# Kernel optimization log

Hardware: AMD Instinct MI355X
Metric: run time of the kernel (lower is better)

Reference implementation:

```python
import jax, jax.numpy as jnp
import numpy as np

N_ROLES = 6
EPS = 1e-5

def _ln(x, scale, bias):
    m = jnp.mean(x, axis=-1, keepdims=True)
    v = jnp.var(x, axis=-1, keepdims=True)
    return (x - m) * jax.lax.rsqrt(v + EPS) * scale + bias

def setup_inputs() -> dict:
    key = jax.random.key(0)
    ks = jax.random.split(key, 20)
    T, B, D_OBS, H, A = 32, 1024, 256, 512, 32
    inp = {
        'rnn_states': jax.random.normal(ks[0], (B, H), jnp.float32),
        'obs': jax.random.normal(ks[1], (T, B, D_OBS), jnp.float32),
        'resets': jnp.zeros((T, B), jnp.float32),
        'available_actions': jnp.ones((T, B, A), jnp.float32),
        'role_ids': jax.random.randint(ks[2], (T, B), 0, N_ROLES, jnp.int32),
        # feature norm over obs_dim
        'fn_scale': jnp.ones((D_OBS,), jnp.float32),
        'fn_bias': jnp.zeros((D_OBS,), jnp.float32),
        # base MLP: obs_dim->512->512, each followed by LayerNorm
        'W0': jax.random.normal(ks[3], (D_OBS, H), jnp.float32) * 0.02,
        'b0': jnp.zeros((H,), jnp.float32),
        'ln0_scale': jnp.ones((H,), jnp.float32),
        'ln0_bias': jnp.zeros((H,), jnp.float32),
        'W1': jax.random.normal(ks[4], (H, H), jnp.float32) * 0.02,
        'b1': jnp.zeros((H,), jnp.float32),
        'ln1_scale': jnp.ones((H,), jnp.float32),
        'ln1_bias': jnp.zeros((H,), jnp.float32),
        # per-role routes: obs_dim->128->H (stacked over roles)
        'Wr0': jax.random.normal(ks[5], (N_ROLES, D_OBS, 128), jnp.float32) * 0.02,
        'br0': jnp.zeros((N_ROLES, 128), jnp.float32),
        'Wr1': jax.random.normal(ks[6], (N_ROLES, 128, H), jnp.float32) * 0.02,
        'br1': jnp.zeros((N_ROLES, H), jnp.float32),
        # per-role heads: H->64->32->action_dim (stacked over roles)
        'Wh0': jax.random.normal(ks[7], (N_ROLES, H, 64), jnp.float32) * 0.02,
        'bh0': jnp.zeros((N_ROLES, 64), jnp.float32),
        'Wh1': jax.random.normal(ks[8], (N_ROLES, 64, 32), jnp.float32) * 0.02,
        'bh1': jnp.zeros((N_ROLES, 32), jnp.float32),
        'Wh2': jax.random.normal(ks[9], (N_ROLES, 32, A), jnp.float32) * 0.02,
        'bh2': jnp.zeros((N_ROLES, A), jnp.float32),
    }
    return inp

def _gather_by_role(all_values, role_ids):
    # all_values: (K, T, B, F); role_ids: (T, B) -> (T, B, F)
    idx = role_ids[None, :, :, None].astype(jnp.int32)
    return jnp.take_along_axis(all_values, idx, axis=0)[0]

def reference(rnn_states, obs, resets, available_actions, role_ids,
              fn_scale, fn_bias, W0, b0, ln0_scale, ln0_bias,
              W1, b1, ln1_scale, ln1_bias,
              Wr0, br0, Wr1, br1,
              Wh0, bh0, Wh1, bh1, Wh2, bh2):
    # feature normalization on raw obs
    obs_n = _ln(obs, fn_scale, fn_bias)
    # shared base MLP (relu + LayerNorm after each Dense)
    e = _ln(jax.nn.relu(obs_n @ W0 + b0), ln0_scale, ln0_bias)
    e = _ln(jax.nn.relu(e @ W1 + b1), ln1_scale, ln1_bias)
    # per-role pre-GRU residual routes on (normalized) obs
    r = jax.nn.relu(jnp.einsum('tbi,kih->ktbh', obs_n, Wr0) + br0[:, None, None, :])
    r = jax.nn.relu(jnp.einsum('ktbh,kho->ktbo', r, Wr1) + br1[:, None, None, :])
    e = e + _gather_by_role(r, role_ids)
    # no recurrent policy configured: rnn_states pass through
    # per-role heads -> all logits (K, T, B, A)
    h = jax.nn.relu(jnp.einsum('tbh,khf->ktbf', e, Wh0) + bh0[:, None, None, :])
    h = jax.nn.relu(jnp.einsum('ktbf,kfg->ktbg', h, Wh1) + bh1[:, None, None, :])
    all_logits = jnp.einsum('ktbg,kga->ktba', h, Wh2) + bh2[:, None, None, :]
    logits = _gather_by_role(all_logits, role_ids)
    logits = jnp.where(available_actions > 0.5, logits, jnp.full_like(logits, -1e10))
    return rnn_states, logits
```

## Files before the change

### kernel.cpp

```cpp
#include <hip/hip_runtime.h>
#include <stdint.h>

typedef unsigned short u16;
typedef unsigned int u32;

using bf16x8 = __attribute__((ext_vector_type(8))) short;
using f32x4  = __attribute__((ext_vector_type(4))) float;

#define DEVINL __device__ __forceinline__

DEVINL float b2f(u16 u) { return __builtin_bit_cast(float, (u32)u << 16); }
DEVINL u16 f2b(float f) {
  u32 u = __builtin_bit_cast(u32, f);
  u += 0x7FFFu + ((u >> 16) & 1u);
  return (u16)(u >> 16);
}

DEVINL void gll16(const u16* src, u16* dst) {
  __builtin_amdgcn_global_load_lds(
      (const __attribute__((address_space(1))) void*)(uintptr_t)src,
      (__attribute__((address_space(3))) void*)(uintptr_t)dst, 16, 0, 0);
}

#define MFMA __builtin_amdgcn_mfma_f32_16x16x32_bf16
#define NROLE 6

__global__ __launch_bounds__(256) void role_count(
    const int* __restrict__ rid, int* __restrict__ blkCnt)
{
  __shared__ int h[NROLE];
  if (threadIdx.x < NROLE) h[threadIdx.x] = 0;
  __syncthreads();
  atomicAdd(&h[rid[blockIdx.x * 256 + threadIdx.x]], 1);
  __syncthreads();
  if (threadIdx.x < NROLE) blkCnt[blockIdx.x * NROLE + threadIdx.x] = h[threadIdx.x];
}

__global__ __launch_bounds__(256) void fill2(
    const int* __restrict__ rid, const int* __restrict__ blkCnt,
    int* __restrict__ bucket, int* __restrict__ baseArr, int* __restrict__ cntArr)
{
  __shared__ int c[128 * NROLE];
  __shared__ int preArr[NROLE], scnt[NROLE], sbase[NROLE], h[NROLE];
  const int tid = threadIdx.x;
  const int bx = blockIdx.x;
  for (int i = tid; i < 128 * NROLE; i += 256) c[i] = blkCnt[i];
  if (tid < NROLE) h[tid] = 0;
  __syncthreads();
  if (tid < NROLE) {
    int k = tid, run = 0, pre = 0;
    for (int b = 0; b < 128; ++b) { if (b == bx) pre = run; run += c[b * NROLE + k]; }
    scnt[k] = run; preArr[k] = pre;
  }
  __syncthreads();
  if (tid == 0) {
    int r = 0;
    for (int k = 0; k < NROLE; ++k) { sbase[k] = r; r += scnt[k]; }
  }
  __syncthreads();
  if (bx == 0 && tid < NROLE) { baseArr[tid] = sbase[tid]; cntArr[tid] = scnt[tid]; }
  int i = bx * 256 + tid;
  int k = rid[i];
  int pos = atomicAdd(&h[k], 1);
  bucket[sbase[k] + preArr[k] + pos] = i;
}

DEVINL void tp_tile(const float* __restrict__ s, u16* __restrict__ d,
                    int R, int C, int bx, int by, int z)
{
  __shared__ u16 tile[32][33];
  const size_t mstride = (size_t)R * C;
  s += (size_t)z * mstride;
  d += (size_t)z * mstride;
  int r0 = bx * 32, c0 = by * 32;
  int tx = threadIdx.x & 31, ty = threadIdx.x >> 5;
#pragma unroll
  for (int i = 0; i < 32; i += 8)
    tile[ty + i][tx] = f2b(s[(size_t)(r0 + ty + i) * C + (c0 + tx)]);
  __syncthreads();
#pragma unroll
  for (int i = 0; i < 32; i += 8)
    d[(size_t)(c0 + ty + i) * R + (r0 + tx)] = tile[tx][ty + i];
}

__global__ __launch_bounds__(256) void mega0(
    const float* W0, const float* W1, const float* Wr0, const float* Wr1, const float* Wh0,
    u16* W0t, u16* W1t, u16* Wr0t, u16* Wr1t, u16* Wh0t,
    const float* __restrict__ obs, const float* __restrict__ fn_s,
    const float* __restrict__ fn_b, u16* __restrict__ obs_nB,
    const int* __restrict__ bucket,
    const float* __restrict__ rnn, float* __restrict__ outRnn)
{
  int b = blockIdx.x;
  const int tid = threadIdx.x;
  if (b < 1152) {
    if (b < 128)      {            tp_tile(W0, W0t, 256, 512, b % 8,  b / 8, 0); }
    else if (b < 384) { b -= 128;  tp_tile(W1, W1t, 512, 512, b % 16, b / 16, 0); }
    else if (b < 576) { b -= 384;  int t = b / 8;  tp_tile(Wr0, Wr0t, 256, 128, b % 8,  t % 4,  t / 4); }
    else if (b < 960) { b -= 576;  int t = b / 4;  tp_tile(Wr1, Wr1t, 128, 512, b % 4,  t % 16, t / 16); }
    else              { b -= 960;  int t = b / 16; tp_tile(Wh0, Wh0t, 512, 64,  b % 16, t % 2,  t / 2); }
  } else if (b < 3200) {
    b -= 1152;
    const int lane = tid & 63, wave = tid >> 6;
#pragma unroll
    for (int it = 0; it < 4; ++it) {
      int p = b * 16 + wave * 4 + it;
      int g = bucket[p];
      const float* xr = obs + (size_t)g * 256 + lane * 4;
      float x[4] __attribute__((aligned(16)));
      *(float4*)x = *(const float4*)xr;
      float s = 0.f, s2 = 0.f;
#pragma unroll
      for (int q = 0; q < 4; ++q) { s += x[q]; s2 += x[q] * x[q]; }
#pragma unroll
      for (int o = 32; o > 0; o >>= 1) { s += __shfl_xor(s, o, 64); s2 += __shfl_xor(s2, o, 64); }
      float m = s * (1.f / 256.f);
      float v = s2 * (1.f / 256.f) - m * m;
      float inv = rsqrtf(v + 1e-5f);
      u16 yu[4] __attribute__((aligned(8)));
#pragma unroll
      for (int q = 0; q < 4; ++q)
        yu[q] = f2b((x[q] - m) * inv * fn_s[lane * 4 + q] + fn_b[lane * 4 + q]);
      *(uint2*)(obs_nB + (size_t)p * 256 + lane * 4) = *(uint2*)yu;
    }
  } else {
    b -= 3200;
    const float4* src = (const float4*)rnn;
    float4* dst = (float4*)outRnn;
    int base = (b * 256 + tid) * 4;
#pragma unroll
    for (int i = 0; i < 4; ++i) dst[base + i] = src[base + i];
  }
}

template <int K>
__global__ __launch_bounds__(256, 2) void gemm_ln(
    const u16* __restrict__ A, const u16* __restrict__ Bt,
    const float* __restrict__ bias, const float* __restrict__ lnsc,
    const float* __restrict__ lnbi, u16* __restrict__ C)
{
  constexpr int BK = 64, NI = K / BK;
  __shared__ __align__(16) u16 As[2][64 * BK];
  __shared__ float redS[64][4];
  __shared__ float redSS[64][4];
  __shared__ float prm[1536];
  const int tid = threadIdx.x;
  const int rowBase = blockIdx.x * 64;
  const int lane = tid & 63, wave = tid >> 6;
#pragma unroll
  for (int i = tid; i < 512; i += 256) {
    prm[i] = bias[i]; prm[512 + i] = lnsc[i]; prm[1024 + i] = lnbi[i];
  }
  u32 aOff[2];
#pragma unroll
  for (int r = 0; r < 2; ++r) {
    int row = r * 32 + (tid >> 3);
    aOff[r] = (u32)(rowBase + row) * (u32)K + (u32)(((tid & 7) ^ (row & 7)) * 8);
  }
  const int quad = lane >> 4, lm = lane & 15, l7 = lm & 7;
  const int wn = wave * 128;
  u32 bOff[8];
#pragma unroll
  for (int j = 0; j < 8; ++j)
    bOff[j] = (u32)(wn + j * 16 + lm) * (u32)K + (u32)(quad * 8);

  f32x4 acc[4][8] = {};

#pragma unroll
  for (int r = 0; r < 2; ++r)
    gll16(A + aOff[r], &As[0][r * 2048 + wave * 512]);
  bf16x8 bP[8];
#pragma unroll
  for (int j = 0; j < 8; ++j)
    bP[j] = *(const bf16x8*)(Bt + bOff[j]);
  __syncthreads();

  for (int i = 0; i < NI; ++i) {
    const u16* Ab = As[i & 1];
    if (i + 1 < NI) {
#pragma unroll
      for (int r = 0; r < 2; ++r)
        gll16(A + aOff[r] + (i + 1) * BK, &As[(i + 1) & 1][r * 2048 + wave * 512]);
    }
    bf16x8 bN[8];
#pragma unroll
    for (int j = 0; j < 8; ++j)
      bN[j] = *(const bf16x8*)(Bt + bOff[j] + i * BK + 32);
    bf16x8 af[4];
#pragma unroll
    for (int i2 = 0; i2 < 4; ++i2)
      af[i2] = *(const bf16x8*)&Ab[(i2 * 16 + lm) * 64 + ((quad ^ l7) * 8)];
#pragma unroll
    for (int i2 = 0; i2 < 4; ++i2)
#pragma unroll
      for (int j = 0; j < 8; ++j)
        acc[i2][j] = MFMA(af[i2], bP[j], acc[i2][j], 0, 0, 0);
    if (i + 1 < NI) {
#pragma unroll
      for (int j = 0; j < 8; ++j)
        bP[j] = *(const bf16x8*)(Bt + bOff[j] + (i + 1) * BK);
    }
#pragma unroll
    for (int i2 = 0; i2 < 4; ++i2)
      af[i2] = *(const bf16x8*)&Ab[(i2 * 16 + lm) * 64 + (((quad + 4) ^ l7) * 8)];
#pragma unroll
    for (int i2 = 0; i2 < 4; ++i2)
#pragma unroll
      for (int j = 0; j < 8; ++j)
        acc[i2][j] = MFMA(af[i2], bN[j], acc[i2][j], 0, 0, 0);
    __syncthreads();
  }

#pragma unroll
  for (int i2 = 0; i2 < 4; ++i2) {
#pragma unroll
    for (int r2 = 0; r2 < 4; ++r2) {
      float s = 0.f, ss = 0.f;
#pragma unroll
      for (int j = 0; j < 8; ++j) {
        float v = fmaxf(acc[i2][j][r2] + prm[wn + j * 16 + lm], 0.f);
        acc[i2][j][r2] = v;
        s += v; ss += v * v;
      }
#pragma unroll
      for (int o = 1; o < 16; o <<= 1) { s += __shfl_xor(s, o, 64); ss += __shfl_xor(ss, o, 64); }
      if (lm == 0) {
        int rowL = i2 * 16 + quad * 4 + r2;
        redS[rowL][wave] = s;
        redSS[rowL][wave] = ss;
      }
    }
  }
  __syncthreads();
#pragma unroll
  for (int i2 = 0; i2 < 4; ++i2) {
#pragma unroll
    for (int r2 = 0; r2 < 4; ++r2) {
      int rowL = i2 * 16 + quad * 4 + r2;
      float ts  = redS[rowL][0] + redS[rowL][1] + redS[rowL][2] + redS[rowL][3];
      float tss = redSS[rowL][0] + redSS[rowL][1] + redSS[rowL][2] + redSS[rowL][3];
      float m = ts * (1.f / 512.f);
      float var = tss * (1.f / 512.f) - m * m;
      float inv = rsqrtf(var + 1e-5f);
      size_t base = (size_t)(rowBase + rowL) * 512;
#pragma unroll
      for (int j = 0; j < 8; ++j) {
        int col = wn + j * 16 + lm;
        float y = (acc[i2][j][r2] - m) * inv * prm[512 + col] + prm[1024 + col];
        C[base + col] = f2b(y);
      }
    }
  }
}

__global__ __launch_bounds__(256, 3) void route_head(
    const u16* __restrict__ obs_nB, const u16* __restrict__ e,
    const u16* __restrict__ Wr0t, const float* __restrict__ br0,
    const u16* __restrict__ Wr1t, const float* __restrict__ br1,
    const u16* __restrict__ Wh0t, const float* __restrict__ bh0,
    const float* __restrict__ Wh1, const float* __restrict__ bh1,
    const float* __restrict__ Wh2, const float* __restrict__ bh2,
    const float* __restrict__ avail,
    const int* __restrict__ bucket, const int* __restrict__ baseArr,
    const int* __restrict__ cntArr, float* __restrict__ outLogits)
{
  __shared__ __align__(16) u16 sm[24960];
  __shared__ float prm[704];
  const int tid = threadIdx.x;

  int role = 0, rem = blockIdx.x, cnt;
  for (;;) {
    cnt = cntArr[role];
    int tiles = (cnt + 31) >> 5;
    if (rem < tiles) break;
    rem -= tiles;
    if (++role >= NROLE) return;
  }
  const int limit = cnt;
  const int rowBase = rem * 32;
  const int roleBase = baseArr[role];

  const int lane = tid & 63, wave = tid >> 6;
  const int quad = lane >> 4, lm = lane & 15, l7 = lm & 7;

#pragma unroll
  for (int r = 0; r < 4; ++r) {
    int lrow = r * 8 + (tid >> 5);
    int i = rowBase + lrow;
    if (i >= limit) i = rowBase;
    gll16(obs_nB + (u32)(roleBase + i) * 256u + (u32)(((tid & 31) ^ (lrow & 7)) * 8),
          &sm[16384 + r * 2048 + wave * 512]);
  }
#pragma unroll
  for (int r = 0; r < 8; ++r) {
    int lrow = r * 4 + wave;
    int i = rowBase + lrow;
    if (i >= limit) i = rowBase;
    int chunk = tid & 63;
    int sw = (chunk & 56) | ((chunk ^ lrow) & 7);
    gll16(e + (u32)(roleBase + i) * 512u + (u32)(sw * 8), &sm[r * 2048 + wave * 512]);
  }
  {
    if (tid < 128) prm[tid] = br0[role * 128 + tid];
    for (int i = tid; i < 512; i += 256) prm[128 + i] = br1[role * 512 + i];
    if (tid < 64) prm[640 + tid] = bh0[role * 64 + tid];
  }
  __syncthreads();

  const int wn0 = wave * 32;
  const u16* B0 = Wr0t + (size_t)role * 128 * 256;
  f32x4 acc0[2][2] = {};
  bf16x8 b0R[2][2];
#pragma unroll
  for (int p = 0; p < 2; ++p)
#pragma unroll
    for (int j = 0; j < 2; ++j)
      b0R[p][j] = *(const bf16x8*)(B0 + (u32)(wn0 + j * 16 + lm) * 256u + (u32)(quad * 8 + p * 32));
#pragma unroll
  for (int it = 0; it < 8; ++it) {
    bf16x8 cur0 = b0R[it & 1][0], cur1 = b0R[it & 1][1];
    if (it + 2 < 8) {
#pragma unroll
      for (int j = 0; j < 2; ++j)
        b0R[it & 1][j] = *(const bf16x8*)(B0 + (u32)(wn0 + j * 16 + lm) * 256u + (u32)(quad * 8 + (it + 2) * 32));
    }
    const int kc = it * 4;
    bf16x8 af[2];
#pragma unroll
    for (int i2 = 0; i2 < 2; ++i2)
      af[i2] = *(const bf16x8*)&sm[16384 + (i2 * 16 + lm) * 256 + (((quad + kc) ^ l7) * 8)];
#pragma unroll
    for (int i2 = 0; i2 < 2; ++i2) {
      acc0[i2][0] = MFMA(af[i2], cur0, acc0[i2][0], 0, 0, 0);
      acc0[i2][1] = MFMA(af[i2], cur1, acc0[i2][1], 0, 0, 0);
    }
  }
  __syncthreads();
  u16* r1 = sm + 16384;
#pragma unroll
  for (int i2 = 0; i2 < 2; ++i2) {
#pragma unroll
    for (int r2 = 0; r2 < 4; ++r2) {
      int row = i2 * 16 + quad * 4 + r2;
#pragma unroll
      for (int j = 0; j < 2; ++j) {
        int col = wn0 + j * 16 + lm;
        float v = fmaxf(acc0[i2][j][r2] + prm[col], 0.f);
        r1[row * 128 + (((col >> 3) ^ (row & 7)) * 8) + (col & 7)] = f2b(v);
      }
    }
  }
  __syncthreads();

  const int wn1 = wave * 128;
  const u16* B1 = Wr1t + (size_t)role * 512 * 128;
  f32x4 acc1[2][8] = {};
  bf16x8 b1P[8];
#pragma unroll
  for (int j = 0; j < 8; ++j)
    b1P[j] = *(const bf16x8*)(B1 + (u32)(wn1 + j * 16 + lm) * 128u + (u32)(quad * 8));
#pragma unroll
  for (int kk = 0; kk < 128; kk += 32) {
    bf16x8 b1N[8];
    if (kk + 32 < 128) {
#pragma unroll
      for (int j = 0; j < 8; ++j)
        b1N[j] = *(const bf16x8*)(B1 + (u32)(wn1 + j * 16 + lm) * 128u + (u32)(quad * 8 + kk + 32));
    }
    const int kc = kk >> 3;
    bf16x8 af[2];
#pragma unroll
    for (int i2 = 0; i2 < 2; ++i2)
      af[i2] = *(const bf16x8*)&r1[(i2 * 16 + lm) * 128 + (((quad + kc) ^ l7) * 8)];
#pragma unroll
    for (int i2 = 0; i2 < 2; ++i2)
#pragma unroll
      for (int j = 0; j < 8; ++j)
        acc1[i2][j] = MFMA(af[i2], b1P[j], acc1[i2][j], 0, 0, 0);
    if (kk + 32 < 128) {
#pragma unroll
      for (int j = 0; j < 8; ++j) b1P[j] = b1N[j];
    }
  }
#pragma unroll
  for (int i2 = 0; i2 < 2; ++i2) {
#pragma unroll
    for (int r2 = 0; r2 < 4; ++r2) {
      int row = i2 * 16 + quad * 4 + r2;
#pragma unroll
      for (int j = 0; j < 8; ++j) {
        int col = wn1 + j * 16 + lm;
        int addr = row * 512 + (((col >> 3) ^ (row & 7)) * 8) + (col & 7);
        float v = fmaxf(acc1[i2][j][r2] + prm[128 + col], 0.f) + b2f(sm[addr]);
        sm[addr] = f2b(v);
      }
    }
  }
  __syncthreads();

  const int wn2 = wave * 16;
  const u16* B2 = Wh0t + (size_t)role * 64 * 512;
  f32x4 acc2[2] = {};
  bf16x8 b2R[4];
#pragma unroll
  for (int p = 0; p < 4; ++p)
    b2R[p] = *(const bf16x8*)(B2 + (u32)(wn2 + lm) * 512u + (u32)(quad * 8 + p * 32));
#pragma unroll
  for (int it = 0; it < 16; ++it) {
    bf16x8 cur = b2R[it & 3];
    if (it + 4 < 16)
      b2R[it & 3] = *(const bf16x8*)(B2 + (u32)(wn2 + lm) * 512u + (u32)(quad * 8 + (it + 4) * 32));
    const int kc = it * 4;
    bf16x8 af[2];
#pragma unroll
    for (int i2 = 0; i2 < 2; ++i2)
      af[i2] = *(const bf16x8*)&sm[(i2 * 16 + lm) * 512 + (((quad + kc) ^ l7) * 8)];
#pragma unroll
    for (int i2 = 0; i2 < 2; ++i2)
      acc2[i2] = MFMA(af[i2], cur, acc2[i2], 0, 0, 0);
  }
  u16* h0s = sm + 20480;
#pragma unroll
  for (int i2 = 0; i2 < 2; ++i2) {
#pragma unroll
    for (int r2 = 0; r2 < 4; ++r2) {
      int row = i2 * 16 + quad * 4 + r2;
      int col = wn2 + lm;
      h0s[row * 68 + col] = f2b(fmaxf(acc2[i2][r2] + prm[640 + col], 0.f));
    }
  }
  __syncthreads();

  {
    float* h1s = (float*)&sm[22656];
    const int r = tid >> 3;
    const int n0 = (tid & 7) * 4;
    const bool valid = (rowBase + r) < limit;
    const float* W1k = Wh1 + (size_t)role * 64 * 32;
    const float* W2k = Wh2 + (size_t)role * 32 * 32;
    float4 a1 = *(const float4*)(bh1 + role * 32 + n0);
#pragma unroll 8
    for (int j = 0; j < 64; ++j) {
      float hj = b2f(h0s[r * 68 + j]);
      float4 wv = *(const float4*)(W1k + j * 32 + n0);
      a1.x += hj * wv.x; a1.y += hj * wv.y; a1.z += hj * wv.z; a1.w += hj * wv.w;
    }
    h1s[r * 36 + n0 + 0] = fmaxf(a1.x, 0.f);
    h1s[r * 36 + n0 + 1] = fmaxf(a1.y, 0.f);
    h1s[r * 36 + n0 + 2] = fmaxf(a1.z, 0.f);
    h1s[r * 36 + n0 + 3] = fmaxf(a1.w, 0.f);
    __syncthreads();
    float4 a2 = *(const float4*)(bh2 + role * 32 + n0);
#pragma unroll 8
    for (int n = 0; n < 32; ++n) {
      float hn = h1s[r * 36 + n];
      float4 wv = *(const float4*)(W2k + n * 32 + n0);
      a2.x += hn * wv.x; a2.y += hn * wv.y; a2.z += hn * wv.z; a2.w += hn * wv.w;
    }
    if (valid) {
      int g = bucket[roleBase + rowBase + r];
      float4 av = *(const float4*)(avail + (size_t)g * 32 + n0);
      float4 o;
      o.x = (av.x > 0.5f) ? a2.x : -1e10f;
      o.y = (av.y > 0.5f) ? a2.y : -1e10f;
      o.z = (av.z > 0.5f) ? a2.z : -1e10f;
      o.w = (av.w > 0.5f) ? a2.w : -1e10f;
      *(float4*)(outLogits + (size_t)g * 32 + n0) = o;
    }
  }
}

extern "C" void kernel_launch(void* const* d_in, const int* in_sizes, int n_in,
                              void* d_out, int out_size, void* d_ws, size_t ws_size,
                              hipStream_t stream)
{
  const float* rnn  = (const float*)d_in[0];
  const float* obs  = (const float*)d_in[1];
  const float* avail= (const float*)d_in[3];
  const int*   rid  = (const int*)d_in[4];
  const float* fn_s = (const float*)d_in[5];
  const float* fn_b = (const float*)d_in[6];
  const float* W0   = (const float*)d_in[7];
  const float* b0   = (const float*)d_in[8];
  const float* ln0s = (const float*)d_in[9];
  const float* ln0b = (const float*)d_in[10];
  const float* W1   = (const float*)d_in[11];
  const float* b1   = (const float*)d_in[12];
  const float* ln1s = (const float*)d_in[13];
  const float* ln1b = (const float*)d_in[14];
  const float* Wr0  = (const float*)d_in[15];
  const float* br0  = (const float*)d_in[16];
  const float* Wr1  = (const float*)d_in[17];
  const float* br1  = (const float*)d_in[18];
  const float* Wh0  = (const float*)d_in[19];
  const float* bh0  = (const float*)d_in[20];
  const float* Wh1  = (const float*)d_in[21];
  const float* bh1  = (const float*)d_in[22];
  const float* Wh2  = (const float*)d_in[23];
  const float* bh2  = (const float*)d_in[24];

  const int ROWS = 32768;

  char* w = (char*)d_ws;
  auto carve = [&](size_t bytes) { char* p = w; w += (bytes + 255) & ~(size_t)255; return p; };
  u16* obs_nB = (u16*)carve((size_t)ROWS * 256 * 2);
  u16* bufA   = (u16*)carve((size_t)ROWS * 512 * 2);
  u16* bufB   = (u16*)carve((size_t)ROWS * 512 * 2);
  u16* W0t    = (u16*)carve((size_t)512 * 256 * 2);
  u16* W1t    = (u16*)carve((size_t)512 * 512 * 2);
  u16* Wr0t   = (u16*)carve((size_t)6 * 128 * 256 * 2);
  u16* Wr1t   = (u16*)carve((size_t)6 * 512 * 128 * 2);
  u16* Wh0t   = (u16*)carve((size_t)6 * 64 * 512 * 2);
  int* bucket = (int*)carve((size_t)ROWS * 4);
  int* blkCnt = (int*)carve((size_t)128 * NROLE * 4);
  int* baseArr= (int*)carve(256);
  int* cntArr = (int*)carve(256);

  float* outLogits = (float*)d_out + (size_t)1024 * 512;

  role_count<<<128, 256, 0, stream>>>(rid, blkCnt);
  fill2<<<128, 256, 0, stream>>>(rid, blkCnt, bucket, baseArr, cntArr);

  mega0<<<3328, 256, 0, stream>>>(W0, W1, Wr0, Wr1, Wh0, W0t, W1t, Wr0t, Wr1t, Wh0t,
                                  obs, fn_s, fn_b, obs_nB, bucket, rnn, (float*)d_out);

  gemm_ln<256><<<512, 256, 0, stream>>>(obs_nB, W0t, b0, ln0s, ln0b, bufA);
  gemm_ln<512><<<512, 256, 0, stream>>>(bufA, W1t, b1, ln1s, ln1b, bufB);

  route_head<<<1029, 256, 0, stream>>>(obs_nB, bufB, Wr0t, br0, Wr1t, br1, Wh0t, bh0,
                                       Wh1, bh1, Wh2, bh2, avail,
                                       bucket, baseArr, cntArr, outLogits);
}
```

Measured before the change: 270.0 us.

## Pad role buckets to 64 rows and split fused route/head into MFMA tile kernels

```diff
diff --git a/kernel.cpp b/kernel.cpp
--- a/kernel.cpp
+++ b/kernel.cpp
@@ -24,6 +24,8 @@
 
 #define MFMA __builtin_amdgcn_mfma_f32_16x16x32_bf16
 #define NROLE 6
+#define PROWS 33152
+#define PBLK  518
 
 __global__ __launch_bounds__(256) void role_count(
     const int* __restrict__ rid, int* __restrict__ blkCnt)
@@ -38,10 +40,10 @@
 
 __global__ __launch_bounds__(256) void fill2(
     const int* __restrict__ rid, const int* __restrict__ blkCnt,
-    int* __restrict__ bucket, int* __restrict__ baseArr, int* __restrict__ cntArr)
+    int* __restrict__ bucket, int* __restrict__ pbaseOut, int* __restrict__ cntArr)
 {
   __shared__ int c[128 * NROLE];
-  __shared__ int preArr[NROLE], scnt[NROLE], sbase[NROLE], h[NROLE];
+  __shared__ int preArr[NROLE], scnt[NROLE], pb[NROLE + 1], h[NROLE];
   const int tid = threadIdx.x;
   const int bx = blockIdx.x;
   for (int i = tid; i < 128 * NROLE; i += 256) c[i] = blkCnt[i];
@@ -54,15 +56,21 @@
   }
   __syncthreads();
   if (tid == 0) {
-    int r = 0;
-    for (int k = 0; k < NROLE; ++k) { sbase[k] = r; r += scnt[k]; }
-  }
-  __syncthreads();
-  if (bx == 0 && tid < NROLE) { baseArr[tid] = sbase[tid]; cntArr[tid] = scnt[tid]; }
+    pb[0] = 0;
+    for (int k = 0; k < NROLE; ++k) pb[k + 1] = pb[k] + ((scnt[k] + 63) & ~63);
+  }
+  __syncthreads();
+  if (bx == 0) {
+    if (tid <= NROLE) pbaseOut[tid] = pb[tid];
+    if (tid < NROLE) cntArr[tid] = scnt[tid];
+    for (int k = 0; k < NROLE; ++k)
+      for (int p = pb[k] + scnt[k] + tid; p < pb[k + 1]; p += 256) bucket[p] = 0;
+    for (int p = pb[NROLE] + tid; p < PROWS; p += 256) bucket[p] = 0;
+  }
   int i = bx * 256 + tid;
   int k = rid[i];
   int pos = atomicAdd(&h[k], 1);
-  bucket[sbase[k] + preArr[k] + pos] = i;
+  bucket[pb[k] + preArr[k] + pos] = i;
 }
 
 DEVINL void tp_tile(const float* __restrict__ s, u16* __restrict__ d,
@@ -99,7 +107,7 @@
     else if (b < 576) { b -= 384;  int t = b / 8;  tp_tile(Wr0, Wr0t, 256, 128, b % 8,  t % 4,  t / 4); }
     else if (b < 960) { b -= 576;  int t = b / 4;  tp_tile(Wr1, Wr1t, 128, 512, b % 4,  t % 16, t / 16); }
     else              { b -= 960;  int t = b / 16; tp_tile(Wh0, Wh0t, 512, 64,  b % 16, t % 2,  t / 2); }
-  } else if (b < 3200) {
+  } else if (b < 1152 + PROWS / 16) {
     b -= 1152;
     const int lane = tid & 63, wave = tid >> 6;
 #pragma unroll
@@ -124,7 +132,7 @@
       *(uint2*)(obs_nB + (size_t)p * 256 + lane * 4) = *(uint2*)yu;
     }
   } else {
-    b -= 3200;
+    b -= 1152 + PROWS / 16;
     const float4* src = (const float4*)rnn;
     float4* dst = (float4*)outRnn;
     int base = (b * 256 + tid) * 4;
@@ -134,10 +142,10 @@
 }
 
 template <int K>
-__global__ __launch_bounds__(256, 2) void gemm_ln(
+DEVINL void gemm_ln_body(
     const u16* __restrict__ A, const u16* __restrict__ Bt,
     const float* __restrict__ bias, const float* __restrict__ lnsc,
-    const float* __restrict__ lnbi, u16* __restrict__ C)
+    const float* __restrict__ lnbi, u16* __restrict__ C, int bx)
 {
   constexpr int BK = 64, NI = K / BK;
   __shared__ __align__(16) u16 As[2][64 * BK];
@@ -145,7 +153,7 @@
   __shared__ float redSS[64][4];
   __shared__ float prm[1536];
   const int tid = threadIdx.x;
-  const int rowBase = blockIdx.x * 64;
+  const int rowBase = bx * 64;
   const int lane = tid & 63, wave = tid >> 6;
 #pragma unroll
   for (int i = tid; i < 512; i += 256) {
@@ -253,219 +261,323 @@
   }
 }
 
-__global__ __launch_bounds__(256, 3) void route_head(
-    const u16* __restrict__ obs_nB, const u16* __restrict__ e,
+DEVINL void route0_body(
+    const u16* __restrict__ A, const u16* __restrict__ Wr0t,
+    const float* __restrict__ br0, u16* __restrict__ r1out,
+    const int* __restrict__ pbase, int bx)
+{
+  constexpr int K = 256, NI = 4;
+  __shared__ __align__(16) u16 As0[2][64 * 64];
+  const int tid = threadIdx.x;
+  const int rowBase = bx * 64;
+  if (rowBase >= pbase[NROLE]) return;
+  int role = 0;
+  while (rowBase >= pbase[role + 1]) ++role;
+  const int lane = tid & 63, wave = tid >> 6;
+  const int quad = lane >> 4, lm = lane & 15, l7 = lm & 7;
+  u32 aOff[2];
+#pragma unroll
+  for (int r = 0; r < 2; ++r) {
+    int row = r * 32 + (tid >> 3);
+    aOff[r] = (u32)(rowBase + row) * (u32)K + (u32)(((tid & 7) ^ (row & 7)) * 8);
+  }
+  const int wn0 = wave * 32;
+  const u16* B0 = Wr0t + (size_t)role * 128 * 256;
+  u32 bOff[2];
+#pragma unroll
+  for (int j = 0; j < 2; ++j)
+    bOff[j] = (u32)(wn0 + j * 16 + lm) * (u32)K + (u32)(quad * 8);
+
+  f32x4 acc[4][2] = {};
+#pragma unroll
+  for (int r = 0; r < 2; ++r)
+    gll16(A + aOff[r], &As0[0][r * 2048 + wave * 512]);
+  bf16x8 bP[2];
+#pragma unroll
+  for (int j = 0; j < 2; ++j) bP[j] = *(const bf16x8*)(B0 + bOff[j]);
+  __syncthreads();
+
+  for (int i = 0; i < NI; ++i) {
+    const u16* Ab = As0[i & 1];
+    if (i + 1 < NI) {
+#pragma unroll
+      for (int r = 0; r < 2; ++r)
+        gll16(A + aOff[r] + (i + 1) * 64, &As0[(i + 1) & 1][r * 2048 + wave * 512]);
+    }
+    bf16x8 bN[2];
+#pragma unroll
+    for (int j = 0; j < 2; ++j) bN[j] = *(const bf16x8*)(B0 + bOff[j] + i * 64 + 32);
+    bf16x8 af[4];
+#pragma unroll
+    for (int i2 = 0; i2 < 4; ++i2)
+      af[i2] = *(const bf16x8*)&Ab[(i2 * 16 + lm) * 64 + ((quad ^ l7) * 8)];
+#pragma unroll
+    for (int i2 = 0; i2 < 4; ++i2)
+#pragma unroll
+      for (int j = 0; j < 2; ++j)
+        acc[i2][j] = MFMA(af[i2], bP[j], acc[i2][j], 0, 0, 0);
+    if (i + 1 < NI) {
+#pragma unroll
+      for (int j = 0; j < 2; ++j) bP[j] = *(const bf16x8*)(B0 + bOff[j] + (i + 1) * 64);
+    }
+#pragma unroll
+    for (int i2 = 0; i2 < 4; ++i2)
+      af[i2] = *(const bf16x8*)&Ab[(i2 * 16 + lm) * 64 + (((quad + 4) ^ l7) * 8)];
+#pragma unroll
+    for (int i2 = 0; i2 < 4; ++i2)
+#pragma unroll
+      for (int j = 0; j < 2; ++j)
+        acc[i2][j] = MFMA(af[i2], bN[j], acc[i2][j], 0, 0, 0);
+    __syncthreads();
+  }
+  float bia[2];
+#pragma unroll
+  for (int j = 0; j < 2; ++j) bia[j] = br0[role * 128 + wn0 + j * 16 + lm];
+#pragma unroll
+  for (int i2 = 0; i2 < 4; ++i2) {
+#pragma unroll
+    for (int r2 = 0; r2 < 4; ++r2) {
+      int row = rowBase + i2 * 16 + quad * 4 + r2;
+#pragma unroll
+      for (int j = 0; j < 2; ++j) {
+        int col = wn0 + j * 16 + lm;
+        r1out[(size_t)row * 128 + col] = f2b(fmaxf(acc[i2][j][r2] + bia[j], 0.f));
+      }
+    }
+  }
+}
+
+__global__ __launch_bounds__(256, 2) void g256_r0(
+    const u16* __restrict__ obs_nB, const u16* __restrict__ W0t,
+    const float* __restrict__ b0, const float* __restrict__ ln0s,
+    const float* __restrict__ ln0b, u16* __restrict__ bufA,
     const u16* __restrict__ Wr0t, const float* __restrict__ br0,
-    const u16* __restrict__ Wr1t, const float* __restrict__ br1,
-    const u16* __restrict__ Wh0t, const float* __restrict__ bh0,
+    u16* __restrict__ r1out, const int* __restrict__ pbase)
+{
+  if (blockIdx.x < PBLK)
+    gemm_ln_body<256>(obs_nB, W0t, b0, ln0s, ln0b, bufA, blockIdx.x);
+  else
+    route0_body(obs_nB, Wr0t, br0, r1out, pbase, blockIdx.x - PBLK);
+}
+
+__global__ __launch_bounds__(256, 2) void gemm512(
+    const u16* __restrict__ bufA, const u16* __restrict__ W1t,
+    const float* __restrict__ b1, const float* __restrict__ ln1s,
+    const float* __restrict__ ln1b, u16* __restrict__ bufB)
+{
+  gemm_ln_body<512>(bufA, W1t, b1, ln1s, ln1b, bufB, blockIdx.x);
+}
+
+__global__ __launch_bounds__(256, 2) void route1_k(
+    const u16* __restrict__ r1, const u16* __restrict__ Wr1t,
+    const float* __restrict__ br1, const u16* __restrict__ e,
+    u16* __restrict__ ea, const int* __restrict__ pbase)
+{
+  constexpr int K = 128, NI = 2;
+  __shared__ __align__(16) u16 As[2][64 * 64];
+  const int tid = threadIdx.x;
+  const int rowBase = blockIdx.x * 64;
+  if (rowBase >= pbase[NROLE]) return;
+  int role = 0;
+  while (rowBase >= pbase[role + 1]) ++role;
+  const int lane = tid & 63, wave = tid >> 6;
+  const int quad = lane >> 4, lm = lane & 15, l7 = lm & 7;
+  u32 aOff[2];
+#pragma unroll
+  for (int r = 0; r < 2; ++r) {
+    int row = r * 32 + (tid >> 3);
+    aOff[r] = (u32)(rowBase + row) * (u32)K + (u32)(((tid & 7) ^ (row & 7)) * 8);
+  }
+  const int wn = wave * 128;
+  const u16* B1 = Wr1t + (size_t)role * 512 * 128;
+  u32 bOff[8];
+#pragma unroll
+  for (int j = 0; j < 8; ++j)
+    bOff[j] = (u32)(wn + j * 16 + lm) * (u32)K + (u32)(quad * 8);
+
+  f32x4 acc[4][8] = {};
+#pragma unroll
+  for (int r = 0; r < 2; ++r)
+    gll16(r1 + aOff[r], &As[0][r * 2048 + wave * 512]);
+  bf16x8 bP[8];
+#pragma unroll
+  for (int j = 0; j < 8; ++j) bP[j] = *(const bf16x8*)(B1 + bOff[j]);
+  __syncthreads();
+
+  for (int i = 0; i < NI; ++i) {
+    const u16* Ab = As[i & 1];
+    if (i + 1 < NI) {
+#pragma unroll
+      for (int r = 0; r < 2; ++r)
+        gll16(r1 + aOff[r] + (i + 1) * 64, &As[(i + 1) & 1][r * 2048 + wave * 512]);
+    }
+    bf16x8 bN[8];
+#pragma unroll
+    for (int j = 0; j < 8; ++j) bN[j] = *(const bf16x8*)(B1 + bOff[j] + i * 64 + 32);
+    bf16x8 af[4];
+#pragma unroll
+    for (int i2 = 0; i2 < 4; ++i2)
+      af[i2] = *(const bf16x8*)&Ab[(i2 * 16 + lm) * 64 + ((quad ^ l7) * 8)];
+#pragma unroll
+    for (int i2 = 0; i2 < 4; ++i2)
+#pragma unroll
+      for (int j = 0; j < 8; ++j)
+        acc[i2][j] = MFMA(af[i2], bP[j], acc[i2][j], 0, 0, 0);
+    if (i + 1 < NI) {
+#pragma unroll
+      for (int j = 0; j < 8; ++j) bP[j] = *(const bf16x8*)(B1 + bOff[j] + (i + 1) * 64);
+    }
+#pragma unroll
+    for (int i2 = 0; i2 < 4; ++i2)
+      af[i2] = *(const bf16x8*)&Ab[(i2 * 16 + lm) * 64 + (((quad + 4) ^ l7) * 8)];
+#pragma unroll
+    for (int i2 = 0; i2 < 4; ++i2)
+#pragma unroll
+      for (int j = 0; j < 8; ++j)
+        acc[i2][j] = MFMA(af[i2], bN[j], acc[i2][j], 0, 0, 0);
+    __syncthreads();
+  }
+  float bia[8];
+#pragma unroll
+  for (int j = 0; j < 8; ++j) bia[j] = br1[role * 512 + wn + j * 16 + lm];
+#pragma unroll
+  for (int i2 = 0; i2 < 4; ++i2) {
+#pragma unroll
+    for (int r2 = 0; r2 < 4; ++r2) {
+      size_t row = (size_t)(rowBase + i2 * 16 + quad * 4 + r2);
+#pragma unroll
+      for (int j = 0; j < 8; ++j) {
+        int col = wn + j * 16 + lm;
+        float v = fmaxf(acc[i2][j][r2] + bia[j], 0.f) + b2f(e[row * 512 + col]);
+        ea[row * 512 + col] = f2b(v);
+      }
+    }
+  }
+}
+
+__global__ __launch_bounds__(256, 2) void head_all(
+    const u16* __restrict__ ea, const u16* __restrict__ Wh0t,
+    const float* __restrict__ bh0,
     const float* __restrict__ Wh1, const float* __restrict__ bh1,
     const float* __restrict__ Wh2, const float* __restrict__ bh2,
-    const float* __restrict__ avail,
-    const int* __restrict__ bucket, const int* __restrict__ baseArr,
-    const int* __restrict__ cntArr, float* __restrict__ outLogits)
-{
-  __shared__ __align__(16) u16 sm[24960];
-  __shared__ float prm[704];
+    const float* __restrict__ avail, const int* __restrict__ bucket,
+    const int* __restrict__ pbase, const int* __restrict__ cntArr,
+    float* __restrict__ outLogits)
+{
+  constexpr int K = 512, NI = 8;
+  __shared__ __align__(16) u16 As[2][64 * 64];
+  __shared__ u16 h0s[64 * 68];
+  __shared__ float h1s[64 * 36];
   const int tid = threadIdx.x;
-
-  int role = 0, rem = blockIdx.x, cnt;
-  for (;;) {
-    cnt = cntArr[role];
-    int tiles = (cnt + 31) >> 5;
-    if (rem < tiles) break;
-    rem -= tiles;
-    if (++role >= NROLE) return;
-  }
-  const int limit = cnt;
-  const int rowBase = rem * 32;
-  const int roleBase = baseArr[role];
-
+  const int rowBase = blockIdx.x * 64;
+  if (rowBase >= pbase[NROLE]) return;
+  int role = 0;
+  while (rowBase >= pbase[role + 1]) ++role;
   const int lane = tid & 63, wave = tid >> 6;
   const int quad = lane >> 4, lm = lane & 15, l7 = lm & 7;
-
-#pragma unroll
-  for (int r = 0; r < 4; ++r) {
-    int lrow = r * 8 + (tid >> 5);
-    int i = rowBase + lrow;
-    if (i >= limit) i = rowBase;
-    gll16(obs_nB + (u32)(roleBase + i) * 256u + (u32)(((tid & 31) ^ (lrow & 7)) * 8),
-          &sm[16384 + r * 2048 + wave * 512]);
-  }
-#pragma unroll
-  for (int r = 0; r < 8; ++r) {
-    int lrow = r * 4 + wave;
-    int i = rowBase + lrow;
-    if (i >= limit) i = rowBase;
-    int chunk = tid & 63;
-    int sw = (chunk & 56) | ((chunk ^ lrow) & 7);
-    gll16(e + (u32)(roleBase + i) * 512u + (u32)(sw * 8), &sm[r * 2048 + wave * 512]);
+  u32 aOff[2];
+#pragma unroll
+  for (int r = 0; r < 2; ++r) {
+    int row = r * 32 + (tid >> 3);
+    aOff[r] = (u32)(rowBase + row) * (u32)K + (u32)(((tid & 7) ^ (row & 7)) * 8);
+  }
+  const int col0 = wave * 16 + lm;
+  const u16* B2 = Wh0t + (size_t)role * 64 * 512;
+  const u32 bOff = (u32)col0 * (u32)K + (u32)(quad * 8);
+
+  f32x4 acc[4] = {};
+#pragma unroll
+  for (int r = 0; r < 2; ++r)
+    gll16(ea + aOff[r], &As[0][r * 2048 + wave * 512]);
+  bf16x8 bP = *(const bf16x8*)(B2 + bOff);
+  __syncthreads();
+
+  for (int i = 0; i < NI; ++i) {
+    const u16* Ab = As[i & 1];
+    if (i + 1 < NI) {
+#pragma unroll
+      for (int r = 0; r < 2; ++r)
+        gll16(ea + aOff[r] + (i + 1) * 64, &As[(i + 1) & 1][r * 2048 + wave * 512]);
+    }
+    bf16x8 bN = *(const bf16x8*)(B2 + bOff + i * 64 + 32);
+    bf16x8 af[4];
+#pragma unroll
+    for (int i2 = 0; i2 < 4; ++i2)
+      af[i2] = *(const bf16x8*)&Ab[(i2 * 16 + lm) * 64 + ((quad ^ l7) * 8)];
+#pragma unroll
+    for (int i2 = 0; i2 < 4; ++i2)
+      acc[i2] = MFMA(af[i2], bP, acc[i2], 0, 0, 0);
+    if (i + 1 < NI) bP = *(const bf16x8*)(B2 + bOff + (i + 1) * 64);
+#pragma unroll
+    for (int i2 = 0; i2 < 4; ++i2)
+      af[i2] = *(const bf16x8*)&Ab[(i2 * 16 + lm) * 64 + (((quad + 4) ^ l7) * 8)];
+#pragma unroll
+    for (int i2 = 0; i2 < 4; ++i2)
+      acc[i2] = MFMA(af[i2], bN, acc[i2], 0, 0, 0);
+    __syncthreads();
   }
   {
-    if (tid < 128) prm[tid] = br0[role * 128 + tid];
-    for (int i = tid; i < 512; i += 256) prm[128 + i] = br1[role * 512 + i];
-    if (tid < 64) prm[640 + tid] = bh0[role * 64 + tid];
-  }
-  __syncthreads();
-
-  const int wn0 = wave * 32;
-  const u16* B0 = Wr0t + (size_t)role * 128 * 256;
-  f32x4 acc0[2][2] = {};
-  bf16x8 b0R[2][2];
-#pragma unroll
-  for (int p = 0; p < 2; ++p)
-#pragma unroll
-    for (int j = 0; j < 2; ++j)
-      b0R[p][j] = *(const bf16x8*)(B0 + (u32)(wn0 + j * 16 + lm) * 256u + (u32)(quad * 8 + p * 32));
-#pragma unroll
-  for (int it = 0; it < 8; ++it) {
-    bf16x8 cur0 = b0R[it & 1][0], cur1 = b0R[it & 1][1];
-    if (it + 2 < 8) {
-#pragma unroll
-      for (int j = 0; j < 2; ++j)
-        b0R[it & 1][j] = *(const bf16x8*)(B0 + (u32)(wn0 + j * 16 + lm) * 256u + (u32)(quad * 8 + (it + 2) * 32));
-    }
-    const int kc = it * 4;
-    bf16x8 af[2];
-#pragma unroll
-    for (int i2 = 0; i2 < 2; ++i2)
-      af[i2] = *(const bf16x8*)&sm[16384 + (i2 * 16 + lm) * 256 + (((quad + kc) ^ l7) * 8)];
-#pragma unroll
-    for (int i2 = 0; i2 < 2; ++i2) {
-      acc0[i2][0] = MFMA(af[i2], cur0, acc0[i2][0], 0, 0, 0);
-      acc0[i2][1] = MFMA(af[i2], cur1, acc0[i2][1], 0, 0, 0);
-    }
-  }
-  __syncthreads();
-  u16* r1 = sm + 16384;
-#pragma unroll
-  for (int i2 = 0; i2 < 2; ++i2) {
-#pragma unroll
-    for (int r2 = 0; r2 < 4; ++r2) {
-      int row = i2 * 16 + quad * 4 + r2;
-#pragma unroll
-      for (int j = 0; j < 2; ++j) {
-        int col = wn0 + j * 16 + lm;
-        float v = fmaxf(acc0[i2][j][r2] + prm[col], 0.f);
-        r1[row * 128 + (((col >> 3) ^ (row & 7)) * 8) + (col & 7)] = f2b(v);
+    float b2v = bh0[role * 64 + col0];
+#pragma unroll
+    for (int i2 = 0; i2 < 4; ++i2)
+#pragma unroll
+      for (int r2 = 0; r2 < 4; ++r2) {
+        int row = i2 * 16 + quad * 4 + r2;
+        h0s[row * 68 + col0] = f2b(fmaxf(acc[i2][r2] + b2v, 0.f));
       }
-    }
-  }
-  __syncthreads();
-
-  const int wn1 = wave * 128;
-  const u16* B1 = Wr1t + (size_t)role * 512 * 128;
-  f32x4 acc1[2][8] = {};
-  bf16x8 b1P[8];
-#pragma unroll
-  for (int j = 0; j < 8; ++j)
-    b1P[j] = *(const bf16x8*)(B1 + (u32)(wn1 + j * 16 + lm) * 128u + (u32)(quad * 8));
-#pragma unroll
-  for (int kk = 0; kk < 128; kk += 32) {
-    bf16x8 b1N[8];
-    if (kk + 32 < 128) {
-#pragma unroll
-      for (int j = 0; j < 8; ++j)
-        b1N[j] = *(const bf16x8*)(B1 + (u32)(wn1 + j * 16 + lm) * 128u + (u32)(quad * 8 + kk + 32));
-    }
-    const int kc = kk >> 3;
-    bf16x8 af[2];
-#pragma unroll
-    for (int i2 = 0; i2 < 2; ++i2)
-      af[i2] = *(const bf16x8*)&r1[(i2 * 16 + lm) * 128 + (((quad + kc) ^ l7) * 8)];
-#pragma unroll
-    for (int i2 = 0; i2 < 2; ++i2)
-#pragma unroll
-      for (int j = 0; j < 8; ++j)
-        acc1[i2][j] = MFMA(af[i2], b1P[j], acc1[i2][j], 0, 0, 0);
-    if (kk + 32 < 128) {
-#pragma unroll
-      for (int j = 0; j < 8; ++j) b1P[j] = b1N[j];
-    }
-  }
-#pragma unroll
-  for (int i2 = 0; i2 < 2; ++i2) {
-#pragma unroll
-    for (int r2 = 0; r2 < 4; ++r2) {
-      int row = i2 * 16 + quad * 4 + r2;
-#pragma unroll
-      for (int j = 0; j < 8; ++j) {
-        int col = wn1 + j * 16 + lm;
-        int addr = row * 512 + (((col >> 3) ^ (row & 7)) * 8) + (col & 7);
-        float v = fmaxf(acc1[i2][j][r2] + prm[128 + col], 0.f) + b2f(sm[addr]);
-        sm[addr] = f2b(v);
-      }
-    }
-  }
-  __syncthreads();
-
-  const int wn2 = wave * 16;
-  const u16* B2 = Wh0t + (size_t)role * 64 * 512;
-  f32x4 acc2[2] = {};
-  bf16x8 b2R[4];
-#pragma unroll
-  for (int p = 0; p < 4; ++p)
-    b2R[p] = *(const bf16x8*)(B2 + (u32)(wn2 + lm) * 512u + (u32)(quad * 8 + p * 32));
-#pragma unroll
-  for (int it = 0; it < 16; ++it) {
-    bf16x8 cur = b2R[it & 3];
-    if (it + 4 < 16)
-      b2R[it & 3] = *(const bf16x8*)(B2 + (u32)(wn2 + lm) * 512u + (u32)(quad * 8 + (it + 4) * 32));
-    const int kc = it * 4;
-    bf16x8 af[2];
-#pragma unroll
-    for (int i2 = 0; i2 < 2; ++i2)
-      af[i2] = *(const bf16x8*)&sm[(i2 * 16 + lm) * 512 + (((quad + kc) ^ l7) * 8)];
-#pragma unroll
-    for (int i2 = 0; i2 < 2; ++i2)
-      acc2[i2] = MFMA(af[i2], cur, acc2[i2], 0, 0, 0);
-  }
-  u16* h0s = sm + 20480;
-#pragma unroll
-  for (int i2 = 0; i2 < 2; ++i2) {
-#pragma unroll
-    for (int r2 = 0; r2 < 4; ++r2) {
-      int row = i2 * 16 + quad * 4 + r2;
-      int col = wn2 + lm;
-      h0s[row * 68 + col] = f2b(fmaxf(acc2[i2][r2] + prm[640 + col], 0.f));
-    }
   }
   __syncthreads();
 
   {
-    float* h1s = (float*)&sm[22656];
-    const int r = tid >> 3;
-    const int n0 = (tid & 7) * 4;
-    const bool valid = (rowBase + r) < limit;
+    const int r = tid >> 2;
+    const int n0 = (tid & 3) * 8;
     const float* W1k = Wh1 + (size_t)role * 64 * 32;
     const float* W2k = Wh2 + (size_t)role * 32 * 32;
-    float4 a1 = *(const float4*)(bh1 + role * 32 + n0);
+    float4 a1a = *(const float4*)(bh1 + role * 32 + n0);
+    float4 a1b = *(const float4*)(bh1 + role * 32 + n0 + 4);
 #pragma unroll 8
     for (int j = 0; j < 64; ++j) {
       float hj = b2f(h0s[r * 68 + j]);
-      float4 wv = *(const float4*)(W1k + j * 32 + n0);
-      a1.x += hj * wv.x; a1.y += hj * wv.y; a1.z += hj * wv.z; a1.w += hj * wv.w;
-    }
-    h1s[r * 36 + n0 + 0] = fmaxf(a1.x, 0.f);
-    h1s[r * 36 + n0 + 1] = fmaxf(a1.y, 0.f);
-    h1s[r * 36 + n0 + 2] = fmaxf(a1.z, 0.f);
-    h1s[r * 36 + n0 + 3] = fmaxf(a1.w, 0.f);
+      float4 wa = *(const float4*)(W1k + j * 32 + n0);
+      float4 wb = *(const float4*)(W1k + j * 32 + n0 + 4);
+      a1a.x += hj * wa.x; a1a.y += hj * wa.y; a1a.z += hj * wa.z; a1a.w += hj * wa.w;
+      a1b.x += hj * wb.x; a1b.y += hj * wb.y; a1b.z += hj * wb.z; a1b.w += hj * wb.w;
+    }
+    h1s[r * 36 + n0 + 0] = fmaxf(a1a.x, 0.f);
+    h1s[r * 36 + n0 + 1] = fmaxf(a1a.y, 0.f);
+    h1s[r * 36 + n0 + 2] = fmaxf(a1a.z, 0.f);
+    h1s[r * 36 + n0 + 3] = fmaxf(a1a.w, 0.f);
+    h1s[r * 36 + n0 + 4] = fmaxf(a1b.x, 0.f);
+    h1s[r * 36 + n0 + 5] = fmaxf(a1b.y, 0.f);
+    h1s[r * 36 + n0 + 6] = fmaxf(a1b.z, 0.f);
+    h1s[r * 36 + n0 + 7] = fmaxf(a1b.w, 0.f);
     __syncthreads();
-    float4 a2 = *(const float4*)(bh2 + role * 32 + n0);
+    float4 a2a = *(const float4*)(bh2 + role * 32 + n0);
+    float4 a2b = *(const float4*)(bh2 + role * 32 + n0 + 4);
 #pragma unroll 8
     for (int n = 0; n < 32; ++n) {
       float hn = h1s[r * 36 + n];
-      float4 wv = *(const float4*)(W2k + n * 32 + n0);
-      a2.x += hn * wv.x; a2.y += hn * wv.y; a2.z += hn * wv.z; a2.w += hn * wv.w;
-    }
-    if (valid) {
-      int g = bucket[roleBase + rowBase + r];
-      float4 av = *(const float4*)(avail + (size_t)g * 32 + n0);
-      float4 o;
-      o.x = (av.x > 0.5f) ? a2.x : -1e10f;
-      o.y = (av.y > 0.5f) ? a2.y : -1e10f;
-      o.z = (av.z > 0.5f) ? a2.z : -1e10f;
-      o.w = (av.w > 0.5f) ? a2.w : -1e10f;
-      *(float4*)(outLogits + (size_t)g * 32 + n0) = o;
+      float4 wa = *(const float4*)(W2k + n * 32 + n0);
+      float4 wb = *(const float4*)(W2k + n * 32 + n0 + 4);
+      a2a.x += hn * wa.x; a2a.y += hn * wa.y; a2a.z += hn * wa.z; a2a.w += hn * wa.w;
+      a2b.x += hn * wb.x; a2b.y += hn * wb.y; a2b.z += hn * wb.z; a2b.w += hn * wb.w;
+    }
+    int local = rowBase + r - pbase[role];
+    if (local < cntArr[role]) {
+      int g = bucket[rowBase + r];
+      float4 ava = *(const float4*)(avail + (size_t)g * 32 + n0);
+      float4 avb = *(const float4*)(avail + (size_t)g * 32 + n0 + 4);
+      float4 oa, ob;
+      oa.x = (ava.x > 0.5f) ? a2a.x : -1e10f;
+      oa.y = (ava.y > 0.5f) ? a2a.y : -1e10f;
+      oa.z = (ava.z > 0.5f) ? a2a.z : -1e10f;
+      oa.w = (ava.w > 0.5f) ? a2a.w : -1e10f;
+      ob.x = (avb.x > 0.5f) ? a2b.x : -1e10f;
+      ob.y = (avb.y > 0.5f) ? a2b.y : -1e10f;
+      ob.z = (avb.z > 0.5f) ? a2b.z : -1e10f;
+      ob.w = (avb.w > 0.5f) ? a2b.w : -1e10f;
+      *(float4*)(outLogits + (size_t)g * 32 + n0) = oa;
+      *(float4*)(outLogits + (size_t)g * 32 + n0 + 4) = ob;
     }
   }
 }
@@ -499,35 +611,38 @@
   const float* Wh2  = (const float*)d_in[23];
   const float* bh2  = (const float*)d_in[24];
 
-  const int ROWS = 32768;
-
   char* w = (char*)d_ws;
   auto carve = [&](size_t bytes) { char* p = w; w += (bytes + 255) & ~(size_t)255; return p; };
-  u16* obs_nB = (u16*)carve((size_t)ROWS * 256 * 2);
-  u16* bufA   = (u16*)carve((size_t)ROWS * 512 * 2);
-  u16* bufB   = (u16*)carve((size_t)ROWS * 512 * 2);
+  u16* obs_nB = (u16*)carve((size_t)PROWS * 256 * 2);
+  u16* bufA   = (u16*)carve((size_t)PROWS * 512 * 2);
+  u16* bufB   = (u16*)carve((size_t)PROWS * 512 * 2);
+  u16* r1buf  = (u16*)carve((size_t)PROWS * 128 * 2);
   u16* W0t    = (u16*)carve((size_t)512 * 256 * 2);
   u16* W1t    = (u16*)carve((size_t)512 * 512 * 2);
   u16* Wr0t   = (u16*)carve((size_t)6 * 128 * 256 * 2);
   u16* Wr1t   = (u16*)carve((size_t)6 * 512 * 128 * 2);
   u16* Wh0t   = (u16*)carve((size_t)6 * 64 * 512 * 2);
-  int* bucket = (int*)carve((size_t)ROWS * 4);
+  int* bucket = (int*)carve((size_t)PROWS * 4);
   int* blkCnt = (int*)carve((size_t)128 * NROLE * 4);
-  int* baseArr= (int*)carve(256);
+  int* pbase  = (int*)carve(256);
   int* cntArr = (int*)carve(256);
 
   float* outLogits = (float*)d_out + (size_t)1024 * 512;
 
   role_count<<<128, 256, 0, stream>>>(rid, blkCnt);
-  fill2<<<128, 256, 0, stream>>>(rid, blkCnt, bucket, baseArr, cntArr);
-
-  mega0<<<3328, 256, 0, stream>>>(W0, W1, Wr0, Wr1, Wh0, W0t, W1t, Wr0t, Wr1t, Wh0t,
-                                  obs, fn_s, fn_b, obs_nB, bucket, rnn, (float*)d_out);
-
-  gemm_ln<256><<<512, 256, 0, stream>>>(obs_nB, W0t, b0, ln0s, ln0b, bufA);
-  gemm_ln<512><<<512, 256, 0, stream>>>(bufA, W1t, b1, ln1s, ln1b, bufB);
-
-  route_head<<<1029, 256, 0, stream>>>(obs_nB, bufB, Wr0t, br0, Wr1t, br1, Wh0t, bh0,
-                                       Wh1, bh1, Wh2, bh2, avail,
-                                       bucket, baseArr, cntArr, outLogits);
-}
+  fill2<<<128, 256, 0, stream>>>(rid, blkCnt, bucket, pbase, cntArr);
+
+  mega0<<<1152 + PROWS / 16 + 128, 256, 0, stream>>>(
+      W0, W1, Wr0, Wr1, Wh0, W0t, W1t, Wr0t, Wr1t, Wh0t,
+      obs, fn_s, fn_b, obs_nB, bucket, rnn, (float*)d_out);
+
+  g256_r0<<<2 * PBLK, 256, 0, stream>>>(obs_nB, W0t, b0, ln0s, ln0b, bufA,
+                                        Wr0t, br0, r1buf, pbase);
+
+  gemm512<<<PBLK, 256, 0, stream>>>(bufA, W1t, b1, ln1s, ln1b, bufB);
+
+  route1_k<<<PBLK, 256, 0, stream>>>(r1buf, Wr1t, br1, bufB, bufA, pbase);
+
+  head_all<<<PBLK, 256, 0, stream>>>(bufA, Wh0t, bh0, Wh1, bh1, Wh2, bh2,
+                                     avail, bucket, pbase, cntArr, outLogits);
+}
```

After: 301.3 us. +11.6%, slower.
